# Kernel tuning notes

Hardware: AMD Instinct MI355X
Metric: run time of the kernel (lower is better)

The kernel has to match this reference:

```python
import jax, jax.numpy as jnp
import numpy as np

B, S, T = 32, 128, 64
V, E, H = 32000, 256, 512


def setup_inputs() -> dict:
    key = jax.random.key(0)
    ks = jax.random.split(key, 32)
    n = jax.random.normal

    def lin(k, fi, fo):
        kw, kb = jax.random.split(k)
        s = 1.0 / np.sqrt(fi)
        return (jax.random.uniform(kw, (fi, fo), jnp.float32, -s, s),
                jax.random.uniform(kb, (fo,), jnp.float32, -s, s))

    W_enc, b_enc = lin(ks[4], 2 * H, H)      # attention.enc_h_in
    W_prev, b_prev = lin(ks[5], H, H)        # attention.prev_s_in
    W_att, b_att = lin(ks[6], H, 1)          # attention.linear
    Wi_g, bi_g = lin(ks[7], E, 2 * H)        # cell.input_weights
    Wh_g, bh_g = lin(ks[8], H, 2 * H)        # cell.hidden_weights
    Wc_g, bc_g = lin(ks[9], 2 * H, 2 * H)    # cell.ctx_weights
    Wi, bi = lin(ks[10], E, H)               # cell.input_in
    Wh, bh = lin(ks[11], H, H)               # cell.hidden_in
    Wc, bc = lin(ks[12], 2 * H, H)           # cell.ctx_in
    W_out, b_out = lin(ks[13], H, V)         # dec2word

    return dict(
        content=n(ks[0], (B, H), jnp.float32),
        sentiment=n(ks[1], (B, H), jnp.float32),
        hiddens=n(ks[2], (B, S, 2 * H), jnp.float32),
        target=jax.random.randint(ks[3], (B, T), 0, V, jnp.int32),
        embed=n(ks[14], (V, E), jnp.float32) * 0.02,
        W_enc=W_enc, b_enc=b_enc, W_prev=W_prev, b_prev=b_prev,
        W_att=W_att, b_att=b_att,
        Wi_g=Wi_g, bi_g=bi_g, Wh_g=Wh_g, bh_g=bh_g, Wc_g=Wc_g, bc_g=bc_g,
        Wi=Wi, bi=bi, Wh=Wh, bh=bh, Wc=Wc, bc=bc,
        W_out=W_out, b_out=b_out,
    )


def reference(content, sentiment, hiddens, target, embed,
              W_enc, b_enc, W_prev, b_prev, W_att, b_att,
              Wi_g, bi_g, Wh_g, bh_g, Wc_g, bc_g,
              Wi, bi, Wh, bh, Wc, bc, W_out, b_out):
    tgt_emb = embed[target]                       # [B, T, E]
    enc_proj = hiddens @ W_enc + b_enc            # [B, S, H], timestep-invariant

    def step(prev_s, x_t):
        # additive attention
        q = prev_s @ W_prev + b_prev              # [B, H]
        h = jnp.tanh(enc_proj + q[:, None, :])    # [B, S, H]
        score = h @ W_att + b_att                 # [B, S, 1]
        alpha = jax.nn.softmax(score, axis=1)     # over source positions
        ctx = jnp.einsum('bsi,bsh->bh', alpha, hiddens)  # [B, 2H]
        # GRU-like cell (original uses only the first gate, as written)
        gates = x_t @ Wi_g + bi_g + prev_s @ Wh_g + bh_g + ctx @ Wc_g + bc_g
        reset_gate, _update_gate = jnp.split(gates, 2, axis=1)
        r = jax.nn.sigmoid(reset_gate)
        s_tilde = jnp.tanh(x_t @ Wi + bi + prev_s @ Wh + bh + ctx @ Wc + bc)
        new_s = (1.0 - r) * prev_s + r * s_tilde
        return new_s, new_s

    _, dec_h = jax.lax.scan(step, content, jnp.swapaxes(tgt_emb, 0, 1))
    dec_h = jnp.swapaxes(dec_h, 0, 1)             # [B, T, H]
    style_logits = sentiment @ W_out + b_out      # [B, V], same every step
    outputs = (dec_h @ W_out + b_out) + 0.5 * style_logits[:, None, :]
    return outputs                                # [B, T, V]
```

## Files before the change

### kernel.cpp

```cpp
#include <hip/hip_runtime.h>
#include <hip/hip_bf16.h>
#include <math.h>

#define NB 32
#define NS 128
#define NT 64
#define NV 32000
#define NE 256
#define NH 512

typedef short s16x8 __attribute__((ext_vector_type(8)));
typedef float f32x4 __attribute__((ext_vector_type(4)));
typedef unsigned u32x4 __attribute__((ext_vector_type(4)));

__device__ __forceinline__ unsigned short f2bf(float x) {
    union { float f; unsigned u; } v; v.f = x;
    unsigned r = v.u + 0x7FFFu + ((v.u >> 16) & 1u);
    return (unsigned short)(r >> 16);
}
__device__ __forceinline__ float bf2f(short h) {
    union { unsigned u; float f; } x;
    x.u = ((unsigned)(unsigned short)h) << 16;
    return x.f;
}

__device__ __forceinline__ void bar_lgkm() {
    asm volatile("s_waitcnt lgkmcnt(0)" ::: "memory");
    __builtin_amdgcn_sched_barrier(0);
    __builtin_amdgcn_s_barrier();
    __builtin_amdgcn_sched_barrier(0);
}

__device__ __forceinline__ void st_pt(unsigned long long* p, unsigned pay, unsigned tag) {
    unsigned long long v = (unsigned long long)pay | ((unsigned long long)tag << 32);
    asm volatile("global_store_dwordx2 %0, %1, off sc0 sc1" :: "v"(p), "v"(v) : "memory");
}
__device__ __forceinline__ void st_coh32(unsigned* p, unsigned v) {
    asm volatile("global_store_dword %0, %1, off sc0 sc1" :: "v"(p), "v"(v) : "memory");
}
__device__ __forceinline__ unsigned ld_coh32(const unsigned* p) {
    unsigned v;
    asm volatile("global_load_dword %0, %1, off sc0 sc1\n\ts_waitcnt vmcnt(0)"
                 : "=v"(v) : "v"(p) : "memory");
    return v;
}
__device__ __forceinline__ void st_coh_x4(void* p, u32x4 v) {
    asm volatile("global_store_dwordx4 %0, %1, off sc0 sc1" :: "v"(p), "v"(v) : "memory");
}
__device__ __forceinline__ void ld64_coh(const void* p, u32x4& a, u32x4& b, u32x4& c, u32x4& d) {
    asm volatile(
        "global_load_dwordx4 %0, %4, off sc0 sc1\n\t"
        "global_load_dwordx4 %1, %4, off offset:16 sc0 sc1\n\t"
        "global_load_dwordx4 %2, %4, off offset:32 sc0 sc1\n\t"
        "global_load_dwordx4 %3, %4, off offset:48 sc0 sc1\n\t"
        "s_waitcnt vmcnt(0)"
        : "=&v"(a), "=&v"(b), "=&v"(c), "=&v"(d)
        : "v"(p) : "memory");
}
__device__ __forceinline__ void ld8_pt(const unsigned long long* b0, unsigned long long* v) {
    unsigned long long v0, v1, v2, v3, v4, v5, v6, v7;
    asm volatile(
        "global_load_dwordx2 %0, %8, off sc0 sc1\n\t"
        "global_load_dwordx2 %1, %9, off sc0 sc1\n\t"
        "global_load_dwordx2 %2, %10, off sc0 sc1\n\t"
        "global_load_dwordx2 %3, %11, off sc0 sc1\n\t"
        "global_load_dwordx2 %4, %12, off sc0 sc1\n\t"
        "global_load_dwordx2 %5, %13, off sc0 sc1\n\t"
        "global_load_dwordx2 %6, %14, off sc0 sc1\n\t"
        "global_load_dwordx2 %7, %15, off sc0 sc1\n\t"
        "s_waitcnt vmcnt(0)"
        : "=&v"(v0), "=&v"(v1), "=&v"(v2), "=&v"(v3),
          "=&v"(v4), "=&v"(v5), "=&v"(v6), "=&v"(v7)
        : "v"(b0), "v"(b0 + 1024), "v"(b0 + 2048), "v"(b0 + 3072),
          "v"(b0 + 4096), "v"(b0 + 5120), "v"(b0 + 6144), "v"(b0 + 7168)
        : "memory");
    v[0] = v0; v[1] = v1; v[2] = v2; v[3] = v3;
    v[4] = v4; v[5] = v5; v[6] = v6; v[7] = v7;
}
__device__ __forceinline__ void ld3_pt(const unsigned long long* p0,
                                       const unsigned long long* p1,
                                       const unsigned long long* p2,
                                       unsigned long long& a, unsigned long long& b,
                                       unsigned long long& c) {
    asm volatile(
        "global_load_dwordx2 %0, %3, off sc0 sc1\n\t"
        "global_load_dwordx2 %1, %4, off sc0 sc1\n\t"
        "global_load_dwordx2 %2, %5, off sc0 sc1\n\t"
        "s_waitcnt vmcnt(0)"
        : "=&v"(a), "=&v"(b), "=&v"(c)
        : "v"(p0), "v"(p1), "v"(p2)
        : "memory");
}

__global__ void build_wfrag_k(const float* __restrict__ Wp,
                              const float* __restrict__ Whg,
                              const float* __restrict__ Wh,
                              unsigned short* __restrict__ wfrag) {
    int blk = blockIdx.x;
    int lane = threadIdx.x;
    int ct = blk >> 4, kt = blk & 15;
    int c = ct * 16 + (lane & 15);
    int kb = kt * 32 + (lane >> 4) * 8;
    s16x8 v;
#pragma unroll
    for (int j = 0; j < 8; ++j) {
        int k = kb + j;
        float x;
        if (c < 512)       x = Wp[k * 512 + c];
        else if (c < 1024) x = Whg[k * 1024 + (c - 512)];
        else               x = Wh[k * 512 + (c - 1024)];
        v[j] = (short)f2bf(x);
    }
    ((s16x8*)wfrag)[blk * 64 + lane] = v;
}

template<int MODE>
__global__ __launch_bounds__(256, 2) void gemm_mfma(
    const float* __restrict__ Af, const unsigned short* __restrict__ Abf,
    const int* __restrict__ gidx,
    const float* __restrict__ B0, const float* __restrict__ B1, const float* __restrict__ B2,
    const float* __restrict__ e0, const float* __restrict__ e1, const float* __restrict__ e2,
    const float* __restrict__ e3, const float* __restrict__ e4, const float* __restrict__ e5,
    void* __restrict__ O0v, void* __restrict__ O1v, void* __restrict__ O2v)
{
    constexpr int M   = (MODE == 0) ? 4096 : 2048;
    constexpr int K   = (MODE == 0) ? 1024 : 256;
    constexpr int LDA = (MODE == 0) ? 1024 : 256;
    constexpr int MB  = M / 128;

    const int bm = blockIdx.x % MB, bn = blockIdx.x / MB;
    const int m0 = bm * 128, n0 = bn * 128;

    const float* Bp; int ldb, coff;
    if constexpr (MODE == 0) {
        int sub = n0 >> 9;
        Bp   = (sub == 0) ? B0 : (sub == 1) ? B1 : B2;
        ldb  = (sub == 1) ? 1024 : 512;
        coff = n0 & 511;
    } else {
        if (n0 < 512) { Bp = B0; ldb = 1024; coff = n0; }
        else          { Bp = B1; ldb = 512;  coff = n0 - 512; }
    }

    __shared__ unsigned short As[128 * 40];
    __shared__ unsigned short Bs[128 * 40];

    const int tid = threadIdx.x, lane = tid & 63, w = tid >> 6;
    const int wr = w >> 1, wc = w & 1;
    const int k0f = (lane >> 4) * 8;
    const int rsel = lane & 15;

    f32x4 acc[4][4];
#pragma unroll
    for (int i = 0; i < 4; ++i)
#pragma unroll
        for (int j = 0; j < 4; ++j) { f32x4 z = {0.f, 0.f, 0.f, 0.f}; acc[i][j] = z; }

    for (int kt = 0; kt < K / 32; ++kt) {
        const int k0 = kt * 32;
        __syncthreads();
#pragma unroll
        for (int i = 0; i < 16; ++i) {
            int idx = tid + i * 256;
            int r = idx >> 5, k = idx & 31;
            unsigned short v;
            if constexpr (MODE == 1) {
                int g = gidx[m0 + r];
                v = f2bf(Af[(size_t)g * 256 + k0 + k]);
            } else {
                v = f2bf(Af[(size_t)(m0 + r) * LDA + k0 + k]);
            }
            As[r * 40 + k] = v;
        }
#pragma unroll
        for (int i = 0; i < 16; ++i) {
            int idx = tid + i * 256;
            int k = idx >> 7, c = idx & 127;
            Bs[c * 40 + k] = f2bf(Bp[(size_t)(k0 + k) * ldb + coff + c]);
        }
        __syncthreads();

        s16x8 af[4], bf[4];
#pragma unroll
        for (int i = 0; i < 4; ++i)
            af[i] = *(const s16x8*)&As[(wr * 64 + i * 16 + rsel) * 40 + k0f];
#pragma unroll
        for (int j = 0; j < 4; ++j)
            bf[j] = *(const s16x8*)&Bs[(wc * 64 + j * 16 + rsel) * 40 + k0f];
#pragma unroll
        for (int i = 0; i < 4; ++i)
#pragma unroll
            for (int j = 0; j < 4; ++j)
                acc[i][j] = __builtin_amdgcn_mfma_f32_16x16x32_bf16(af[i], bf[j], acc[i][j], 0, 0, 0);
    }

    const int rg = (lane >> 4) * 4;
#pragma unroll
    for (int i = 0; i < 4; ++i)
#pragma unroll
        for (int j = 0; j < 4; ++j) {
            int row0 = m0 + wr * 64 + i * 16 + rg;
            int col  = n0 + wc * 64 + j * 16 + rsel;
            if constexpr (MODE == 0) {
                int sub = col >> 9;
                if (sub == 0) {
                    unsigned short* Ta = (unsigned short*)O0v;
#pragma unroll
                    for (int r = 0; r < 4; ++r)
                        Ta[(size_t)(row0 + r) * 512 + col] = f2bf(tanhf(acc[i][j][r] + e0[col]));
                } else {
                    int h = col & 511;
                    int bb = row0 >> 7, s0 = row0 & 127;
                    unsigned long long pk = 0;
#pragma unroll
                    for (int r = 0; r < 4; ++r)
                        pk |= (unsigned long long)f2bf(acc[i][j][r]) << (16 * r);
                    unsigned short* dstp = (sub == 1) ? (unsigned short*)O1v : (unsigned short*)O2v;
                    *(unsigned long long*)&dstp[(size_t)((bb * 512 + h) * 128 + s0)] = pk;
                }
            } else {
                float* Of = (float*)O0v;
                float bias;
                if (col < 512) bias = e0[col] + e1[col] + e2[col];
                else { int h = col - 512; bias = e3[h] + e4[h] + e5[h]; }
#pragma unroll
                for (int r = 0; r < 4; ++r)
                    Of[(size_t)(row0 + r) * 1024 + col] = acc[i][j][r] + bias;
            }
        }
}

__global__ __launch_bounds__(1024) void fused_scan_out(
    const float* __restrict__ content, const float* __restrict__ sentiment,
    const float* __restrict__ b_prev,  const float* __restrict__ W_att,
    const unsigned short* __restrict__ Ta_bf,
    const unsigned short* __restrict__ hWcg_t,
    const unsigned short* __restrict__ hWc_t,
    const float* __restrict__ xgxs, const unsigned short* __restrict__ wfrag,
    unsigned long long* __restrict__ Spl, unsigned long long* __restrict__ Upl,
    unsigned short* __restrict__ dh, unsigned* __restrict__ prog,
    unsigned* __restrict__ packdone, unsigned short* __restrict__ wpk,
    const float* __restrict__ W_out, const float* __restrict__ b_out,
    float* __restrict__ out)
{
    __shared__ __attribute__((aligned(16))) char smem[90624];
    const int tid = threadIdx.x, lane = tid & 63, w = tid >> 6;

    if (blockIdx.x < NB) {
        const int b = blockIdx.x;
        unsigned short* W_lds = (unsigned short*)smem;
        unsigned short* S_lds = (unsigned short*)(smem + 49152);
        float* tq = (float*)(smem + 83456);
        float* sc = (float*)(smem + 85504);
        float* al = (float*)(smem + 86016);
        float* cg = (float*)(smem + 86528);
        float* cs = (float*)(smem + 88576);

        {
            const s16x8* src = (const s16x8*)wfrag + (size_t)b * (3 * 16 * 64);
            s16x8* dst = (s16x8*)W_lds;
            for (int i = tid; i < 3 * 16 * 64; i += 1024) dst[i] = src[i];
        }
        float s_reg = 0.f, senth = 0.f, bprev_h = 0.f;
        if (tid < 512) {
            s_reg   = content[b * 512 + tid];
            senth   = 0.5f * sentiment[b * 512 + tid];
            bprev_h = b_prev[tid];
        }
        float wv[8];
        {
            const f32x4* wa = (const f32x4*)&W_att[lane * 8];
            f32x4 a0 = wa[0], a1 = wa[1];
#pragma unroll
            for (int j = 0; j < 4; ++j) { wv[j] = a0[j]; wv[4 + j] = a1[j]; }
        }
        const int kbase = (lane >> 4) * 8;
        const int mat = tid >> 9, hh = tid & 511;
        const s16x8* Mp = (const s16x8*)((mat ? hWc_t : hWcg_t) + ((size_t)(b * 512 + hh)) * 128);

        if (tid < 512) {
            float nsn = __shfl_down(s_reg, 1, 64);
            if (!(lane & 1)) {
                unsigned pay = (unsigned)f2bf(s_reg) | ((unsigned)f2bf(nsn) << 16);
                st_pt(&Spl[b * 256 + (tid >> 1)], pay, 1u);
            }
        }

        for (int t = 0; t < 64; ++t) {
            const unsigned want = (unsigned)(t + 1);
            float xg_pre = 0.f, xs_pre = 0.f;
            if (tid < 512) {
                xg_pre = xgxs[((size_t)b * 64 + t) * 1024 + tid];
                xs_pre = xgxs[((size_t)b * 64 + t) * 1024 + 512 + tid];
            }

            {
                unsigned long long v[8];
                const unsigned long long* base = &Spl[tid];
                ld8_pt(base, v);
                for (;;) {
                    bool ok = true;
#pragma unroll
                    for (int ii = 0; ii < 8; ++ii) ok &= ((unsigned)(v[ii] >> 32) == want);
                    if (ok) break;
                    __builtin_amdgcn_s_sleep(1);
                    ld8_pt(base, v);
                }
#pragma unroll
                for (int ii = 0; ii < 8; ++ii) {
                    int idx = tid + ii * 1024;
                    int r = idx >> 8, c = (idx & 255) * 2;
                    *(unsigned*)&S_lds[r * 536 + c] = (unsigned)v[ii];
                }
            }
            bar_lgkm();

            if (w < 6) {
                const int mt = w & 1, ct = w >> 1;
                const int arow = mt * 16 + (lane & 15);
                f32x4 ae = {0.f, 0.f, 0.f, 0.f}, ao = {0.f, 0.f, 0.f, 0.f};
                const s16x8* wl = (const s16x8*)W_lds;
#pragma unroll
                for (int kt = 0; kt < 16; kt += 2) {
                    s16x8 a0 = *(const s16x8*)&S_lds[arow * 536 + kt * 32 + kbase];
                    s16x8 a1 = *(const s16x8*)&S_lds[arow * 536 + (kt + 1) * 32 + kbase];
                    ae = __builtin_amdgcn_mfma_f32_16x16x32_bf16(a0, wl[(ct * 16 + kt) * 64 + lane], ae, 0, 0, 0);
                    ao = __builtin_amdgcn_mfma_f32_16x16x32_bf16(a1, wl[(ct * 16 + kt + 1) * 64 + lane], ao, 0, 0, 0);
                }
                f32x4 a4 = ae + ao;
                const int cout = b * 48 + ct * 16 + (lane & 15);
                const int rbase = mt * 16 + (lane >> 4) * 4;
#pragma unroll
                for (int r = 0; r < 4; ++r)
                    st_pt(&Upl[(size_t)(rbase + r) * 1536 + cout], __float_as_uint(a4[r]), want);
            }

            float guv = 0.f, suv = 0.f;
            if (tid < 512) {
                unsigned long long u0, u1, u2;
                const unsigned long long* q0 = &Upl[b * 1536 + tid];
                const unsigned long long* q1 = &Upl[b * 1536 + 512 + tid];
                const unsigned long long* q2 = &Upl[b * 1536 + 1024 + tid];
                ld3_pt(q0, q1, q2, u0, u1, u2);
                while (((unsigned)(u0 >> 32) != want) | ((unsigned)(u1 >> 32) != want) |
                       ((unsigned)(u2 >> 32) != want)) {
                    __builtin_amdgcn_s_sleep(1);
                    ld3_pt(q0, q1, q2, u0, u1, u2);
                }
                float qv = __uint_as_float((unsigned)u0);
                guv = __uint_as_float((unsigned)u1);
                suv = __uint_as_float((unsigned)u2);
                tq[tid] = tanhf(qv + bprev_h);
            }
            bar_lgkm();

            {
                float tqv[8];
                const f32x4* tp = (const f32x4*)&tq[lane * 8];
                f32x4 t0 = tp[0], t1 = tp[1];
#pragma unroll
                for (int j = 0; j < 4; ++j) { tqv[j] = t0[j]; tqv[4 + j] = t1[j]; }
#pragma unroll
                for (int s8 = 0; s8 < 8; ++s8) {
                    int s = w * 8 + s8;
                    s16x8 tv = *(const s16x8*)&Ta_bf[((size_t)(b * 128 + s)) * 512 + lane * 8];
                    float a = 0.f;
#pragma unroll
                    for (int j = 0; j < 8; ++j) {
                        float ta = bf2f(tv[j]);
                        float num = ta + tqv[j];
                        float den = fmaf(ta, tqv[j], 1.0f);
                        a = fmaf(wv[j], num * __builtin_amdgcn_rcpf(den), a);
                    }
#pragma unroll
                    for (int off = 32; off; off >>= 1) a += __shfl_xor(a, off, 64);
                    if (lane == 0) sc[s] = a;
                }
            }
            bar_lgkm();
            if (w == 0) {
                float v0 = sc[lane], v1 = sc[lane + 64];
                float m = fmaxf(v0, v1);
#pragma unroll
                for (int off = 32; off; off >>= 1) m = fmaxf(m, __shfl_xor(m, off, 64));
                float p0 = __expf(v0 - m), p1 = __expf(v1 - m);
                float sm = p0 + p1;
#pragma unroll
                for (int off = 32; off; off >>= 1) sm += __shfl_xor(sm, off, 64);
                float inv = __builtin_amdgcn_rcpf(sm);
                al[lane] = p0 * inv; al[lane + 64] = p1 * inv;
            }
            bar_lgkm();
            {
                float a0 = 0.f, a1 = 0.f;
#pragma unroll
                for (int q = 0; q < 16; ++q) {
                    s16x8 v = Mp[q];
#pragma unroll
                    for (int j = 0; j < 8; j += 2) {
                        a0 = fmaf(al[q * 8 + j],     bf2f(v[j]),     a0);
                        a1 = fmaf(al[q * 8 + j + 1], bf2f(v[j + 1]), a1);
                    }
                }
                if (mat) cs[hh] = a0 + a1; else cg[hh] = a0 + a1;
            }
            bar_lgkm();
            if (tid < 512) {
                int h = tid;
                float g  = guv + xg_pre + cg[h];
                float r  = __builtin_amdgcn_rcpf(1.0f + __expf(-g));
                float sp = suv + xs_pre + cs[h];
                float e  = __expf(2.0f * sp);
                float st = 1.0f - 2.0f * __builtin_amdgcn_rcpf(e + 1.0f);
                float ns = s_reg + r * (st - s_reg);
                s_reg = ns;
                float dv = ns + senth;
                float dvn = __shfl_down(dv, 1, 64);
                if (!(lane & 1)) {
                    unsigned pk = (unsigned)f2bf(dv) | ((unsigned)f2bf(dvn) << 16);
                    st_coh32((unsigned*)dh + ((((size_t)t * 32 + b) * 512 + h) >> 1), pk);
                }
                if (t < 63) {
                    float nsn = __shfl_down(ns, 1, 64);
                    if (!(lane & 1)) {
                        unsigned pay = (unsigned)f2bf(ns) | ((unsigned)f2bf(nsn) << 16);
                        st_pt(&Spl[b * 256 + (h >> 1)], pay, (unsigned)(t + 2));
                    }
                }
            }
            if ((t & 7) == 7) asm volatile("s_waitcnt vmcnt(0)" ::: "memory");
            bar_lgkm();
            if ((t & 7) == 7 && tid == 0)
                st_coh32(&prog[b * 16], (unsigned)(t + 1));
        }
    } else {
        const int k4 = blockIdx.x - NB;
        unsigned short* As = (unsigned short*)smem;

        for (int u = k4 * 16 + w; u < 32000; u += 224 * 16) {
            int ct = u >> 4, kt = u & 15;
            int c = ct * 16 + (lane & 15);
            int kb = kt * 32 + (lane >> 4) * 8;
            s16x8 v;
#pragma unroll
            for (int j = 0; j < 8; ++j)
                v[j] = (short)f2bf(W_out[(size_t)(kb + j) * 32000 + c]);
            union { s16x8 s; u32x4 u4; } cv; cv.s = v;
            st_coh_x4(&wpk[(size_t)u * 512 + (size_t)lane * 8], cv.u4);
        }
        asm volatile("s_waitcnt vmcnt(0)" ::: "memory");
        __syncthreads();
        if (tid == 0)
            __hip_atomic_fetch_add(packdone, 1u, __ATOMIC_RELAXED, __HIP_MEMORY_SCOPE_AGENT);
        if (w == 0 && lane == 0) {
            while (__hip_atomic_load(packdone, __ATOMIC_RELAXED, __HIP_MEMORY_SCOPE_AGENT) < 224u)
                __builtin_amdgcn_s_sleep(16);
        }
        __syncthreads();
        __builtin_amdgcn_fence(__ATOMIC_ACQUIRE, "agent");
        __syncthreads();

        const int wr = w >> 2, wc = w & 3;
        const int k0f = (lane >> 4) * 8;
        const int rsel = lane & 15;
        const int rg = (lane >> 4) * 4;
        const int ar4 = tid >> 2, aq = tid & 3;
        const s16x8* wpk8 = (const s16x8*)wpk;

        for (int idx = k4; idx < 1000; idx += 224) {
            const int tm = idx / 125, tn = idx - tm * 125;
            const unsigned need = (unsigned)(tm * 8 + 8);
            if (w == 0) {
                for (;;) {
                    unsigned v = 0xFFFFFFFFu;
                    if (lane < 32) v = ld_coh32(&prog[lane * 16]);
                    if (__all(v >= need)) break;
                    __builtin_amdgcn_s_sleep(32);
                }
            }
            __syncthreads();

            const int m0 = tm * 256, n0 = tn * 256;
            f32x4 acc[4][4];
#pragma unroll
            for (int i = 0; i < 4; ++i)
#pragma unroll
                for (int j = 0; j < 4; ++j) { f32x4 z = {0.f, 0.f, 0.f, 0.f}; acc[i][j] = z; }

#pragma unroll
            for (int kq = 0; kq < 4; ++kq) {
                __syncthreads();
                {
                    const unsigned short* sp = &dh[(size_t)(m0 + ar4) * 512 + kq * 128 + aq * 32];
                    u32x4 a0, a1, a2, a3;
                    ld64_coh(sp, a0, a1, a2, a3);
                    int base = ar4 * 136 + aq * 32;
                    *(u32x4*)&As[base]      = a0;
                    *(u32x4*)&As[base + 8]  = a1;
                    *(u32x4*)&As[base + 16] = a2;
                    *(u32x4*)&As[base + 24] = a3;
                }
                __syncthreads();
#pragma unroll
                for (int kk = 0; kk < 4; ++kk) {
                    const int kt = kq * 4 + kk;
                    s16x8 bfr[4], af[4];
#pragma unroll
                    for (int j = 0; j < 4; ++j)
                        bfr[j] = wpk8[(size_t)(((tn * 16 + wc * 4 + j) * 16 + kt)) * 64 + lane];
#pragma unroll
                    for (int i = 0; i < 4; ++i)
                        af[i] = *(const s16x8*)&As[(wr * 64 + i * 16 + rsel) * 136 + kk * 32 + k0f];
#pragma unroll
                    for (int i = 0; i < 4; ++i)
#pragma unroll
                        for (int j = 0; j < 4; ++j)
                            acc[i][j] = __builtin_amdgcn_mfma_f32_16x16x32_bf16(af[i], bfr[j], acc[i][j], 0, 0, 0);
                }
            }

#pragma unroll
            for (int i = 0; i < 4; ++i)
#pragma unroll
                for (int j = 0; j < 4; ++j) {
                    int trow0 = m0 + wr * 64 + i * 16 + rg;
                    int col   = n0 + wc * 64 + j * 16 + rsel;
                    float bb_ = 1.5f * b_out[col];
#pragma unroll
                    for (int r = 0; r < 4; ++r) {
                        int trow = trow0 + r;
                        int bb = trow & 31, tt = trow >> 5;
                        out[(size_t)(bb * 64 + tt) * 32000 + col] = acc[i][j][r] + bb_;
                    }
                }
        }
    }
}

extern "C" void kernel_launch(void* const* d_in, const int* in_sizes, int n_in,
                              void* d_out, int out_size, void* d_ws, size_t ws_size,
                              hipStream_t stream) {
    const float* content  = (const float*)d_in[0];
    const float* sentiment= (const float*)d_in[1];
    const float* hiddens  = (const float*)d_in[2];
    const int*   target   = (const int*)  d_in[3];
    const float* embed    = (const float*)d_in[4];
    const float* W_enc = (const float*)d_in[5];  const float* b_enc = (const float*)d_in[6];
    const float* W_prev= (const float*)d_in[7];  const float* b_prev= (const float*)d_in[8];
    const float* W_att = (const float*)d_in[9];
    const float* Wi_g  = (const float*)d_in[11]; const float* bi_g  = (const float*)d_in[12];
    const float* Wh_g  = (const float*)d_in[13]; const float* bh_g  = (const float*)d_in[14];
    const float* Wc_g  = (const float*)d_in[15]; const float* bc_g  = (const float*)d_in[16];
    const float* Wi    = (const float*)d_in[17]; const float* bi    = (const float*)d_in[18];
    const float* Wh    = (const float*)d_in[19]; const float* bh    = (const float*)d_in[20];
    const float* Wc    = (const float*)d_in[21]; const float* bc    = (const float*)d_in[22];
    const float* W_out = (const float*)d_in[23]; const float* b_out = (const float*)d_in[24];
    float* out = (float*)d_out;

    char* ws = (char*)d_ws;
    unsigned short* wfrag = (unsigned short*)ws;
    unsigned long long* Spl = (unsigned long long*)(ws + 0x180000);
    unsigned long long* Upl = (unsigned long long*)(ws + 0x190000);
    unsigned* prog = (unsigned*)(ws + 0x1F0000);
    unsigned* packdone = (unsigned*)(ws + 0x1F0800);
    unsigned short* Ta_bf   = (unsigned short*)(ws + 0x200000);
    unsigned short* hWcg_t  = (unsigned short*)(ws + 0x600000);
    unsigned short* hWc_t   = (unsigned short*)(ws + 0xA00000);
    float* xgxs     = (float*)(ws + 0xE00000);
    unsigned short* dh      = (unsigned short*)(ws + 0x1600000);
    unsigned short* wpk     = (unsigned short*)(ws + 0x1800000);

    hipMemsetAsync(ws + 0x180000, 0, 0x71000, stream);

    build_wfrag_k<<<96 * 16, 64, 0, stream>>>(W_prev, Wh_g, Wh, wfrag);

    gemm_mfma<0><<<32 * 12, 256, 0, stream>>>(
        hiddens, nullptr, nullptr, W_enc, Wc_g, Wc,
        b_enc, nullptr, nullptr, nullptr, nullptr, nullptr,
        (void*)Ta_bf, (void*)hWcg_t, (void*)hWc_t);

    gemm_mfma<1><<<16 * 8, 256, 0, stream>>>(
        embed, nullptr, target, Wi_g, Wi, nullptr,
        bi_g, bh_g, bc_g, bi, bh, bc,
        (void*)xgxs, nullptr, nullptr);

    fused_scan_out<<<256, 1024, 0, stream>>>(
        content, sentiment, b_prev, W_att, Ta_bf, hWcg_t, hWc_t,
        xgxs, wfrag, Spl, Upl, dh, prog, packdone, wpk, W_out, b_out, out);

    (void)in_sizes; (void)n_in; (void)out_size; (void)ws_size;
}
```

Baseline: 1.283 ms.

## Aggregate scan progress into single min counter and reassign output tiles contiguously

One output-GEMM block becomes a monitor that repeatedly reduces the 32 per-batch scan progress counters to a minimum and publishes it to a single word. The other 223 blocks poll that one word instead of each reading 32 counters. Each block now takes a contiguous range of tiles ordered with the M index fastest, so it reuses the same W_out column tile and follows the progress of the timestep scan. This cuts polling traffic on the coherent counters and spreads waiting more evenly, at the cost of one block doing no GEMM work and the extra latency of the monitor hop.

```diff
diff --git a/kernel.cpp b/kernel.cpp
--- a/kernel.cpp
+++ b/kernel.cpp
@@ -239,7 +239,8 @@
     const float* __restrict__ xgxs, const unsigned short* __restrict__ wfrag,
     unsigned long long* __restrict__ Spl, unsigned long long* __restrict__ Upl,
     unsigned short* __restrict__ dh, unsigned* __restrict__ prog,
-    unsigned* __restrict__ packdone, unsigned short* __restrict__ wpk,
+    unsigned* __restrict__ packdone, unsigned* __restrict__ minprog,
+    unsigned short* __restrict__ wpk,
     const float* __restrict__ W_out, const float* __restrict__ b_out,
     float* __restrict__ out)
 {
@@ -452,6 +453,24 @@
         __syncthreads();
         if (tid == 0)
             __hip_atomic_fetch_add(packdone, 1u, __ATOMIC_RELAXED, __HIP_MEMORY_SCOPE_AGENT);
+
+        if (k4 == 0) {
+            if (w == 0) {
+                for (;;) {
+                    unsigned v = 0xFFFFFFFFu;
+                    if (lane < 32) v = ld_coh32(&prog[lane * 16]);
+                    unsigned mn = v;
+#pragma unroll
+                    for (int off = 32; off; off >>= 1)
+                        mn = min(mn, (unsigned)__shfl_xor((int)mn, off, 64));
+                    if (lane == 0) st_coh32(minprog, mn);
+                    if (mn >= 64u) break;
+                    __builtin_amdgcn_s_sleep(4);
+                }
+            }
+            return;
+        }
+
         if (w == 0 && lane == 0) {
             while (__hip_atomic_load(packdone, __ATOMIC_RELAXED, __HIP_MEMORY_SCOPE_AGENT) < 224u)
                 __builtin_amdgcn_s_sleep(16);
@@ -466,17 +485,16 @@
         const int rg = (lane >> 4) * 4;
         const int ar4 = tid >> 2, aq = tid & 3;
         const s16x8* wpk8 = (const s16x8*)wpk;
-
-        for (int idx = k4; idx < 1000; idx += 224) {
-            const int tm = idx / 125, tn = idx - tm * 125;
+        const int c = k4 - 1;
+        const int jstart = (c * 1000) / 223;
+        const int jend   = ((c + 1) * 1000) / 223;
+
+        for (int j = jstart; j < jend; ++j) {
+            const int tn = j >> 3, tm = j & 7;
             const unsigned need = (unsigned)(tm * 8 + 8);
             if (w == 0) {
-                for (;;) {
-                    unsigned v = 0xFFFFFFFFu;
-                    if (lane < 32) v = ld_coh32(&prog[lane * 16]);
-                    if (__all(v >= need)) break;
+                while (ld_coh32(minprog) < need)
                     __builtin_amdgcn_s_sleep(32);
-                }
             }
             __syncthreads();
 
@@ -485,7 +503,7 @@
 #pragma unroll
             for (int i = 0; i < 4; ++i)
 #pragma unroll
-                for (int j = 0; j < 4; ++j) { f32x4 z = {0.f, 0.f, 0.f, 0.f}; acc[i][j] = z; }
+                for (int jj = 0; jj < 4; ++jj) { f32x4 z = {0.f, 0.f, 0.f, 0.f}; acc[i][jj] = z; }
 
 #pragma unroll
             for (int kq = 0; kq < 4; ++kq) {
@@ -506,31 +524,31 @@
                     const int kt = kq * 4 + kk;
                     s16x8 bfr[4], af[4];
 #pragma unroll
-                    for (int j = 0; j < 4; ++j)
-                        bfr[j] = wpk8[(size_t)(((tn * 16 + wc * 4 + j) * 16 + kt)) * 64 + lane];
+                    for (int jj = 0; jj < 4; ++jj)
+                        bfr[jj] = wpk8[(size_t)(((tn * 16 + wc * 4 + jj) * 16 + kt)) * 64 + lane];
 #pragma unroll
                     for (int i = 0; i < 4; ++i)
                         af[i] = *(const s16x8*)&As[(wr * 64 + i * 16 + rsel) * 136 + kk * 32 + k0f];
 #pragma unroll
                     for (int i = 0; i < 4; ++i)
 #pragma unroll
-                        for (int j = 0; j < 4; ++j)
-                            acc[i][j] = __builtin_amdgcn_mfma_f32_16x16x32_bf16(af[i], bfr[j], acc[i][j], 0, 0, 0);
+                        for (int jj = 0; jj < 4; ++jj)
+                            acc[i][jj] = __builtin_amdgcn_mfma_f32_16x16x32_bf16(af[i], bfr[jj], acc[i][jj], 0, 0, 0);
                 }
             }
 
 #pragma unroll
             for (int i = 0; i < 4; ++i)
 #pragma unroll
-                for (int j = 0; j < 4; ++j) {
+                for (int jj = 0; jj < 4; ++jj) {
                     int trow0 = m0 + wr * 64 + i * 16 + rg;
-                    int col   = n0 + wc * 64 + j * 16 + rsel;
+                    int col   = n0 + wc * 64 + jj * 16 + rsel;
                     float bb_ = 1.5f * b_out[col];
 #pragma unroll
                     for (int r = 0; r < 4; ++r) {
                         int trow = trow0 + r;
                         int bb = trow & 31, tt = trow >> 5;
-                        out[(size_t)(bb * 64 + tt) * 32000 + col] = acc[i][j][r] + bb_;
+                        out[(size_t)(bb * 64 + tt) * 32000 + col] = acc[i][jj][r] + bb_;
                     }
                 }
         }
@@ -563,6 +581,7 @@
     unsigned long long* Upl = (unsigned long long*)(ws + 0x190000);
     unsigned* prog = (unsigned*)(ws + 0x1F0000);
     unsigned* packdone = (unsigned*)(ws + 0x1F0800);
+    unsigned* minprog  = (unsigned*)(ws + 0x1F0900);
     unsigned short* Ta_bf   = (unsigned short*)(ws + 0x200000);
     unsigned short* hWcg_t  = (unsigned short*)(ws + 0x600000);
     unsigned short* hWc_t   = (unsigned short*)(ws + 0xA00000);
@@ -586,7 +605,8 @@
 
     fused_scan_out<<<256, 1024, 0, stream>>>(
         content, sentiment, b_prev, W_att, Ta_bf, hWcg_t, hWc_t,
-        xgxs, wfrag, Spl, Upl, dh, prog, packdone, wpk, W_out, b_out, out);
+        xgxs, wfrag, Spl, Upl, dh, prog, packdone, minprog, wpk,
+        W_out, b_out, out);
 
     (void)in_sizes; (void)n_in; (void)out_size; (void)ws_size;
 }
```

Result: slower. 1.376 ms (+7.2%).
